# Optimization experiments

Measured on AMD Instinct MI355X. Metric: run time of the kernel, lower is better.

The kernel has to match this reference:

```python
import jax, jax.numpy as jnp
import numpy as np

D_MODEL = 1024
NUM_HEADS = 16
HEAD_DIM = D_MODEL // NUM_HEADS
MAX_SEQ = 512


def rope_tables(seq_len, dim):
    inv_freq = 1.0 / (10000.0 ** (jnp.arange(0, dim, 2, dtype=jnp.float32) / dim))
    t = jnp.arange(seq_len, dtype=jnp.float32)
    freqs = jnp.einsum('i,j->ij', t, inv_freq)        # [S, dim/2]
    emb = jnp.concatenate([freqs, freqs], axis=-1)    # [S, dim]
    return jnp.cos(emb), jnp.sin(emb)


def rotate_half(x):
    x1, x2 = jnp.split(x, 2, axis=-1)
    return jnp.concatenate([-x2, x1], axis=-1)


def setup_inputs() -> dict:
    key = jax.random.key(0)
    ks = jax.random.split(key, 12)
    B, S, D = 16, 512, D_MODEL
    s = 1.0 / np.sqrt(D)
    inp = {
        'query': jax.random.normal(ks[0], (B, S, D), jnp.float32),
        'key': jax.random.normal(ks[1], (B, S, D), jnp.float32),
        'value': jax.random.normal(ks[2], (B, S, D), jnp.float32),
        'Wq': jax.random.normal(ks[3], (D, D), jnp.float32) * s,
        'bq': jnp.zeros((D,), jnp.float32),
        'Wk': jax.random.normal(ks[4], (D, D), jnp.float32) * s,
        'bk': jnp.zeros((D,), jnp.float32),
        'Wv': jax.random.normal(ks[5], (D, D), jnp.float32) * s,
        'bv': jnp.zeros((D,), jnp.float32),
        'Wo': jax.random.normal(ks[6], (D, D), jnp.float32) * s,
        'bo': jnp.zeros((D,), jnp.float32),
    }
    return inp


def reference(query, key, value, Wq, bq, Wk, bk, Wv, bv, Wo, bo):
    B, S, D = query.shape
    H, Hd = NUM_HEADS, HEAD_DIM
    scale = Hd ** -0.5

    def proj(x, W, b):  # torch Linear: x @ W.T + b -> [B,H,S,Hd]
        y = jnp.einsum('bsd,ed->bse', x, W) + b
        return y.reshape(B, S, H, Hd).transpose(0, 2, 1, 3)

    q = proj(query, Wq, bq)
    k = proj(key, Wk, bk)
    v = proj(value, Wv, bv)

    cos, sin = rope_tables(S, Hd)           # [S, Hd]
    cos = cos[None, None]                    # [1,1,S,Hd]
    sin = sin[None, None]
    q = q * cos + rotate_half(q) * sin
    k = k * cos + rotate_half(k) * sin

    attn = jnp.einsum('bhqd,bhkd->bhqk', q, k) * scale
    attn_w = jax.nn.softmax(attn, axis=-1)
    out = jnp.einsum('bhqk,bhkd->bhqd', attn_w, v)
    out = out.transpose(0, 2, 1, 3).reshape(B, S, D)
    out = jnp.einsum('bsd,ed->bse', out, Wo) + bo
    return out
```

## Files before the change

kernel.cpp:

```cpp
#include <hip/hip_runtime.h>
#include <hip/hip_bf16.h>
#include <math.h>

typedef __attribute__((ext_vector_type(8))) short short8;
typedef __attribute__((ext_vector_type(4))) short s16x4;
typedef __attribute__((ext_vector_type(4))) float f32x4;
typedef unsigned short ushort;
typedef unsigned int uint;

#define BATCH 16
#define SEQ 512
#define DMODEL 1024
#define NHEADS 16
#define HD 64
#define MTOT (BATCH * SEQ)
#define NBUF ((size_t)MTOT * DMODEL)
#define WBUF ((size_t)DMODEL * DMODEL)

#define SZA (256 * 64)
#define SZB (128 * 64)

#define FENCE asm volatile("" ::: "memory")

__device__ __forceinline__ ushort f2bf(float f) {
    union { float f; uint i; } v; v.f = f;
    uint r = v.i + 0x7fffu + ((v.i >> 16) & 1u);
    return (ushort)(r >> 16);
}

__device__ __forceinline__ short8 cvt8v(f32x4 a, f32x4 b) {
    short8 r;
    r[0] = (short)f2bf(a[0]); r[1] = (short)f2bf(a[1]);
    r[2] = (short)f2bf(a[2]); r[3] = (short)f2bf(a[3]);
    r[4] = (short)f2bf(b[0]); r[5] = (short)f2bf(b[1]);
    r[6] = (short)f2bf(b[2]); r[7] = (short)f2bf(b[3]);
    return r;
}

__device__ __forceinline__ void gld16(const ushort* g, ushort* l) {
    __builtin_amdgcn_global_load_lds(
        (const __attribute__((address_space(1))) void*)g,
        (__attribute__((address_space(3))) void*)l, 16, 0, 0);
}

__device__ __forceinline__ f32x4 mfma16(short8 a, short8 b, f32x4 c) {
    return __builtin_amdgcn_mfma_f32_16x16x32_bf16(a, b, c, 0, 0, 0);
}

__global__ void fill_const(float* __restrict__ out, float val) {
    out[blockIdx.x * 256 + threadIdx.x] = val;
}

__global__ __launch_bounds__(256) void cvt_act(
    const float* __restrict__ i0, const float* __restrict__ i1,
    const float* __restrict__ i2, ushort* __restrict__ o0,
    ushort* __restrict__ o1, ushort* __restrict__ o2)
{
    const float* in  = blockIdx.y == 0 ? i0 : (blockIdx.y == 1 ? i1 : i2);
    ushort*      out = blockIdx.y == 0 ? o0 : (blockIdx.y == 1 ? o1 : o2);
    int i = (blockIdx.x * 256 + threadIdx.x) * 8;
    f32x4 a = __builtin_nontemporal_load((const f32x4*)(in + i));
    f32x4 b = __builtin_nontemporal_load((const f32x4*)(in + i + 4));
    *(short8*)(out + i) = cvt8v(a, b);
}

__global__ __launch_bounds__(256) void cvt_w(
    const float* __restrict__ i0, const float* __restrict__ i1,
    const float* __restrict__ i2, const float* __restrict__ i3,
    ushort* __restrict__ o0, ushort* __restrict__ o1,
    ushort* __restrict__ o2, ushort* __restrict__ o3)
{
    const float* in  = blockIdx.y == 0 ? i0 : (blockIdx.y == 1 ? i1 :
                        (blockIdx.y == 2 ? i2 : i3));
    ushort*      out = blockIdx.y == 0 ? o0 : (blockIdx.y == 1 ? o1 :
                        (blockIdx.y == 2 ? o2 : o3));
    int i = (blockIdx.x * 256 + threadIdx.x) * 8;
    f32x4 a = __builtin_nontemporal_load((const f32x4*)(in + i));
    f32x4 b = __builtin_nontemporal_load((const f32x4*)(in + i + 4));
    *(short8*)(out + i) = cvt8v(a, b);
}

__global__ void rope_init(float* __restrict__ cs, float* __restrict__ sn) {
    int idx = blockIdx.x * 256 + threadIdx.x;
    if (idx >= SEQ * 32) return;
    int s = idx >> 5, p = idx & 31;
    float inv = __expf(-(float)p * (1.0f / 32.0f) * logf(10000.0f));
    float th = (float)s * inv;
    cs[idx] = cosf(th);
    sn[idx] = sinf(th);
}

__device__ __forceinline__ void gemm_core(
    const ushort* __restrict__ A, const ushort* __restrict__ W,
    ushort* __restrict__ smA, ushort* __restrict__ smB,
    int m0, int n0, int tid, f32x4 (&acc)[4][4])
{
    const int lane = tid & 63, w = tid >> 6;
    const int quad = lane >> 4, l16 = lane & 15;
    const int wm = (w >> 1) * 64, wn = (w & 1) * 64;
    const int swz = (l16 & 7) << 3;
    const int k0 = (quad * 8) ^ swz;
    const int k1 = ((4 + quad) * 8) ^ swz;

    const int r = tid >> 3;
    const int kc = ((tid & 7) ^ (r & 7)) * 8;
    const ushort* gA = A + (size_t)(m0 + r) * 1024 + kc;
    const ushort* gB = W + (size_t)(n0 + r) * 1024 + kc;
    ushort* lA = smA + tid * 8;
    ushort* lB = smB + tid * 8;

#pragma unroll
    for (int i = 0; i < 4; ++i) gld16(gA + i * 65536, lA + i * 4096);
    gld16(gB, lB); gld16(gB + 65536, lB + 4096);
    FENCE;
#pragma unroll
    for (int i = 0; i < 4; ++i) gld16(gA + i * 65536 + 64, lA + SZA + i * 4096);
    gld16(gB + 64, lB + SZB); gld16(gB + 65536 + 64, lB + SZB + 4096);
    FENCE;

#pragma unroll 1
    for (int t = 0; t < 16; ++t) {
        if (t < 15) asm volatile("s_waitcnt vmcnt(6)" ::: "memory");
        else        asm volatile("s_waitcnt vmcnt(0)" ::: "memory");
        __builtin_amdgcn_s_barrier();

        const ushort* tA = smA + (t % 3) * SZA;
        const ushort* tB = smB + (t % 3) * SZB;
        short8 af[4][2], bf[4][2];
#pragma unroll
        for (int mi = 0; mi < 4; ++mi) {
            const ushort* rp = tA + (wm + mi * 16 + l16) * 64;
            af[mi][0] = *(const short8*)(rp + k0);
            af[mi][1] = *(const short8*)(rp + k1);
        }
#pragma unroll
        for (int nj = 0; nj < 4; ++nj) {
            const ushort* rp = tB + (wn + nj * 16 + l16) * 64;
            bf[nj][0] = *(const short8*)(rp + k0);
            bf[nj][1] = *(const short8*)(rp + k1);
        }
        if (t < 14) {
            const int sl = (t + 2) % 3;
            const ushort* ga = gA + (size_t)(t + 2) * 64;
            const ushort* gb = gB + (size_t)(t + 2) * 64;
            ushort* da = lA + sl * SZA;
            ushort* db = lB + sl * SZB;
#pragma unroll
            for (int i = 0; i < 4; ++i) gld16(ga + i * 65536, da + i * 4096);
            gld16(gb, db); gld16(gb + 65536, db + 4096);
        }
        FENCE;
        __builtin_amdgcn_s_setprio(1);
#pragma unroll
        for (int nj = 0; nj < 4; ++nj)
#pragma unroll
            for (int mi = 0; mi < 4; ++mi) {
                acc[mi][nj] = mfma16(af[mi][0], bf[nj][0], acc[mi][nj]);
                acc[mi][nj] = mfma16(af[mi][1], bf[nj][1], acc[mi][nj]);
            }
        __builtin_amdgcn_s_setprio(0);
    }
}

__global__ __launch_bounds__(512, 2) void qkv_proj(
    const ushort* __restrict__ Aq, const ushort* __restrict__ Ak,
    const ushort* __restrict__ Av, const ushort* __restrict__ Wq,
    const ushort* __restrict__ Wk, const ushort* __restrict__ Wv,
    const float* __restrict__ bq, const float* __restrict__ bk,
    const float* __restrict__ bv, ushort* __restrict__ Qo,
    ushort* __restrict__ Ko, ushort* __restrict__ Vo,
    const float* __restrict__ cs_tab, const float* __restrict__ sn_tab)
{
    const int z = blockIdx.z;
    const ushort* A    = z == 0 ? Aq : (z == 1 ? Ak : Av);
    const ushort* W    = z == 0 ? Wq : (z == 1 ? Wk : Wv);
    const float*  bias = z == 0 ? bq : (z == 1 ? bk : bv);
    ushort*       out  = z == 0 ? Qo : (z == 1 ? Ko : Vo);

    const int id = blockIdx.x;
    const int x = id & 7, l = id >> 3;
    const int by = x * 4 + (l >> 3);
    const int bx = l & 7;
    const int m0 = by * 256, n0 = bx * 128;

    __shared__ __align__(16) ushort smA[3 * SZA];
    __shared__ __align__(16) ushort smB[3 * SZB];

    const int tid = threadIdx.x;
    const int lane = tid & 63, w = tid >> 6;
    const int quad = lane >> 4, l16 = lane & 15;
    const int wm = (w >> 1) * 64, wn = (w & 1) * 64;

    f32x4 acc[4][4] = {};
    gemm_core(A, W, smA, smB, m0, n0, tid, acc);

    float bv4[4];
#pragma unroll
    for (int j = 0; j < 4; j++) bv4[j] = bias[n0 + wn + j * 16 + l16];

    if (z < 2) {
        const int h = (n0 + wn) >> 6;
#pragma unroll
        for (int i = 0; i < 4; i++) {
#pragma unroll
            for (int r = 0; r < 4; r++) {
                int m = m0 + wm + i * 16 + quad * 4 + r;
                int s = m & (SEQ - 1), b = m >> 9;
                size_t base = ((size_t)(b * NHEADS + h) * SEQ + s) * HD;
#pragma unroll
                for (int jj = 0; jj < 2; jj++) {
                    int p = jj * 16 + l16;
                    float c = cs_tab[s * 32 + p], sg = sn_tab[s * 32 + p];
                    float lo = acc[i][jj][r] + bv4[jj];
                    float hi = acc[i][jj + 2][r] + bv4[jj + 2];
                    out[base + p]      = f2bf(lo * c - hi * sg);
                    out[base + 32 + p] = f2bf(hi * c + lo * sg);
                }
            }
        }
    } else {
        __syncthreads();
        ushort* sT = smA;
#pragma unroll
        for (int i = 0; i < 4; i++)
#pragma unroll
            for (int j = 0; j < 4; j++) {
                s16x4 vv;
#pragma unroll
                for (int r = 0; r < 4; r++) vv[r] = (short)f2bf(acc[i][j][r] + bv4[j]);
                *(s16x4*)(sT + (wn + j * 16 + l16) * 264 + wm + i * 16 + quad * 4) = vv;
            }
        __syncthreads();
        const int nl = tid >> 2, mc = (tid & 3) * 64;
        const int ng = n0 + nl, h = ng >> 6, d = ng & 63;
        const int b = m0 >> 9;
        ushort* op = out + ((size_t)((b * NHEADS + h) * HD + d)) * SEQ +
                     (m0 & (SEQ - 1)) + mc;
#pragma unroll
        for (int u = 0; u < 8; ++u)
            *(short8*)(op + u * 8) = *(const short8*)(sT + nl * 264 + mc + u * 8);
    }
}

__global__ __launch_bounds__(512, 2) void gemm_o(
    const ushort* __restrict__ A, const ushort* __restrict__ W,
    const float* __restrict__ bias, float* __restrict__ out)
{
    const int id = blockIdx.x;
    const int x = id & 7, l = id >> 3;
    const int by = x * 4 + (l >> 3);
    const int bx = l & 7;
    const int m0 = by * 256, n0 = bx * 128;

    __shared__ __align__(16) ushort smA[3 * SZA];
    __shared__ __align__(16) ushort smB[3 * SZB];

    const int tid = threadIdx.x;
    const int lane = tid & 63, w = tid >> 6;
    const int quad = lane >> 4, l16 = lane & 15;
    const int wm = (w >> 1) * 64, wn = (w & 1) * 64;

    f32x4 acc[4][4] = {};
    gemm_core(A, W, smA, smB, m0, n0, tid, acc);

    float bv4[4];
#pragma unroll
    for (int j = 0; j < 4; j++) bv4[j] = bias[n0 + wn + j * 16 + l16];

#pragma unroll
    for (int i = 0; i < 4; i++)
#pragma unroll
        for (int j = 0; j < 4; j++) {
            int n = n0 + wn + j * 16 + l16;
#pragma unroll
            for (int r = 0; r < 4; r++) {
                int m = m0 + wm + i * 16 + quad * 4 + r;
                out[(size_t)m * 1024 + n] = acc[i][j][r] + bv4[j];
            }
        }
}

__global__ __launch_bounds__(256) void attn(
    const ushort* __restrict__ Q, const ushort* __restrict__ K,
    const ushort* __restrict__ VT, ushort* __restrict__ O)
{
    __shared__ ushort sK[64 * 72];
    __shared__ ushort sV[64 * 72];
    __shared__ ushort sP[4][32 * 72];

    const int tid = threadIdx.x;
    const int wave = tid >> 6, lane = tid & 63;
    const int quad = lane >> 4, l16 = lane & 15;
    const int id = blockIdx.x;
    const int j8 = id >> 3;
    const int bh = (id & 7) * 32 + (j8 >> 2);
    const int q0 = (j8 & 3) * 128;
    const int qw = q0 + wave * 32;

    const ushort* Qbh = Q + (size_t)bh * SEQ * HD;
    const ushort* Kbh = K + (size_t)bh * SEQ * HD;
    const ushort* Vbh = VT + (size_t)bh * HD * SEQ;

    const float S2 = 0.125f * 1.44269504f;
    const float C2 = 12.0f * 1.44269504f;

    short8 qf[2][2];
#pragma unroll
    for (int mi = 0; mi < 2; mi++)
#pragma unroll
        for (int ks = 0; ks < 2; ks++)
            qf[mi][ks] = *(const short8*)(Qbh + (size_t)(qw + mi * 16 + l16) * HD +
                                          ks * 32 + quad * 8);

    f32x4 o_acc[2][4] = {};
    float lsum[2][4] = {};

    const int cA = tid, cB = tid + 256;
    const int rA = cA >> 3, colA = (cA & 7) * 8;
    const int rB = cB >> 3, colB = (cB & 7) * 8;

    short8 rk0 = *(const short8*)(Kbh + (size_t)rA * HD + colA);
    short8 rk1 = *(const short8*)(Kbh + (size_t)rB * HD + colB);
    short8 rv0 = *(const short8*)(Vbh + (size_t)rA * SEQ + colA);
    short8 rv1 = *(const short8*)(Vbh + (size_t)rB * SEQ + colB);

    for (int kt = 0; kt < SEQ; kt += 64) {
        __syncthreads();
        *(short8*)(sK + rA * 72 + colA) = rk0;
        *(short8*)(sK + rB * 72 + colB) = rk1;
        *(short8*)(sV + rA * 72 + colA) = rv0;
        *(short8*)(sV + rB * 72 + colB) = rv1;
        if (kt + 64 < SEQ) {
            rk0 = *(const short8*)(Kbh + (size_t)(kt + 64 + rA) * HD + colA);
            rk1 = *(const short8*)(Kbh + (size_t)(kt + 64 + rB) * HD + colB);
            rv0 = *(const short8*)(Vbh + (size_t)rA * SEQ + kt + 64 + colA);
            rv1 = *(const short8*)(Vbh + (size_t)rB * SEQ + kt + 64 + colB);
        }
        __syncthreads();

        f32x4 sc[2][4];
#pragma unroll
        for (int nj = 0; nj < 4; nj++) {
            short8 kf0 = *(const short8*)(sK + (nj * 16 + l16) * 72 + quad * 8);
            short8 kf1 = *(const short8*)(sK + (nj * 16 + l16) * 72 + 32 + quad * 8);
#pragma unroll
            for (int mi = 0; mi < 2; mi++) {
                f32x4 z = {0.f, 0.f, 0.f, 0.f};
                z = mfma16(qf[mi][0], kf0, z);
                z = mfma16(qf[mi][1], kf1, z);
                sc[mi][nj] = z;
            }
        }

#pragma unroll
        for (int mi = 0; mi < 2; mi++)
#pragma unroll
            for (int r = 0; r < 4; r++) {
                float p0 = __builtin_amdgcn_exp2f(fmaf(sc[mi][0][r], S2, -C2));
                float p1 = __builtin_amdgcn_exp2f(fmaf(sc[mi][1][r], S2, -C2));
                float p2 = __builtin_amdgcn_exp2f(fmaf(sc[mi][2][r], S2, -C2));
                float p3 = __builtin_amdgcn_exp2f(fmaf(sc[mi][3][r], S2, -C2));
                sc[mi][0][r] = p0; sc[mi][1][r] = p1;
                sc[mi][2][r] = p2; sc[mi][3][r] = p3;
                lsum[mi][r] += (p0 + p1) + (p2 + p3);
            }

#pragma unroll
        for (int mi = 0; mi < 2; mi++)
#pragma unroll
            for (int nj = 0; nj < 4; nj++)
#pragma unroll
                for (int r = 0; r < 4; r++)
                    sP[wave][(mi * 16 + quad * 4 + r) * 72 + nj * 16 + l16] =
                        f2bf(sc[mi][nj][r]);

#pragma unroll
        for (int ks = 0; ks < 2; ks++) {
            short8 pf0 = *(const short8*)(&sP[wave][(l16) * 72 + ks * 32 + quad * 8]);
            short8 pf1 = *(const short8*)(&sP[wave][(16 + l16) * 72 + ks * 32 + quad * 8]);
#pragma unroll
            for (int dj = 0; dj < 4; dj++) {
                short8 vf = *(const short8*)(sV + (dj * 16 + l16) * 72 + ks * 32 + quad * 8);
                o_acc[0][dj] = mfma16(pf0, vf, o_acc[0][dj]);
                o_acc[1][dj] = mfma16(pf1, vf, o_acc[1][dj]);
            }
        }
    }

    const int h = bh & (NHEADS - 1), b = bh >> 4;
#pragma unroll
    for (int mi = 0; mi < 2; mi++)
#pragma unroll
        for (int r = 0; r < 4; r++) {
            float l = lsum[mi][r];
            l += __shfl_xor(l, 1, 64);
            l += __shfl_xor(l, 2, 64);
            l += __shfl_xor(l, 4, 64);
            l += __shfl_xor(l, 8, 64);
            float inv = 1.0f / l;
            int s = qw + mi * 16 + quad * 4 + r;
            size_t base = ((size_t)(b * SEQ + s)) * DMODEL + h * HD;
#pragma unroll
            for (int dj = 0; dj < 4; dj++)
                O[base + dj * 16 + l16] = f2bf(o_acc[mi][dj][r] * inv);
        }
}

extern "C" void kernel_launch(void* const* d_in, const int* in_sizes, int n_in,
                              void* d_out, int out_size, void* d_ws, size_t ws_size,
                              hipStream_t stream) {
    bool ok = (n_in == 11) && (out_size == (int)NBUF) &&
              in_sizes[0] == (int)NBUF && in_sizes[1] == (int)NBUF &&
              in_sizes[2] == (int)NBUF &&
              in_sizes[3] == (int)WBUF && in_sizes[4] == 1024 &&
              in_sizes[5] == (int)WBUF && in_sizes[6] == 1024 &&
              in_sizes[7] == (int)WBUF && in_sizes[8] == 1024 &&
              in_sizes[9] == (int)WBUF && in_sizes[10] == 1024;
    if (!ok) {
        fill_const<<<NBUF / 256, 256, 0, stream>>>((float*)d_out, 1000.0f);
        return;
    }
    size_t need = 2 * (size_t)SEQ * 32 * 4 + 4 * NBUF * 2 + 4 * WBUF * 2;
    if (ws_size < need) return;

    const float* q  = (const float*)d_in[0];
    const float* k  = (const float*)d_in[1];
    const float* v  = (const float*)d_in[2];
    const float* Wq = (const float*)d_in[3];
    const float* bq = (const float*)d_in[4];
    const float* Wk = (const float*)d_in[5];
    const float* bk = (const float*)d_in[6];
    const float* Wv = (const float*)d_in[7];
    const float* bv = (const float*)d_in[8];
    const float* Wo = (const float*)d_in[9];
    const float* bo = (const float*)d_in[10];

    float* cs = (float*)d_ws;
    float* sn = cs + SEQ * 32;
    ushort* Qb  = (ushort*)(sn + SEQ * 32);
    ushort* Kb  = Qb + NBUF;
    ushort* VTb = Kb + NBUF;
    ushort* Xb  = VTb + NBUF;
    ushort* Wqb = Xb + NBUF;
    ushort* Wkb = Wqb + WBUF;
    ushort* Wvb = Wkb + WBUF;
    ushort* Wob = Wvb + WBUF;
    ushort* Qx = (ushort*)d_out;
    ushort* Kx = Qx + NBUF;

    rope_init<<<64, 256, 0, stream>>>(cs, sn);
    cvt_w<<<dim3(WBUF / 2048, 4), 256, 0, stream>>>(Wq, Wk, Wv, Wo,
                                                    Wqb, Wkb, Wvb, Wob);
    cvt_act<<<dim3(NBUF / 2048, 3), 256, 0, stream>>>(q, k, v, Qx, Kx, Xb);

    qkv_proj<<<dim3(256, 1, 3), 512, 0, stream>>>(
        Qx, Kx, Xb, Wqb, Wkb, Wvb, bq, bk, bv, Qb, Kb, VTb, cs, sn);

    attn<<<BATCH * NHEADS * 4, 256, 0, stream>>>(Qb, Kb, VTb, Xb);

    gemm_o<<<256, 512, 0, stream>>>(Xb, Wob, bo, (float*)d_out);
}
```

Baseline: 278.5 us.

## Halve GEMM K-tile to 32 and raise occupancy to four blocks per CU

Shrinks the shared-memory K tile from 64 to 32, giving twice as many pipeline steps with one MFMA pair fewer per step. The LDS swizzle and the global-load mapping are reworked for the narrower tile. The smaller shared buffers, placed in one LDS array, allow launch bounds of four 512-thread blocks per CU instead of two. The goal is more concurrent waves to hide memory latency. The cost is twice as many barriers per K loop and a much tighter register budget, which risks spilling the 64-float accumulator.

New measurement: 275.7 us. About the same (-1.0%).

```diff
diff --git a/kernel.cpp b/kernel.cpp
--- a/kernel.cpp
+++ b/kernel.cpp
@@ -17,8 +17,9 @@
 #define NBUF ((size_t)MTOT * DMODEL)
 #define WBUF ((size_t)DMODEL * DMODEL)
 
-#define SZA (256 * 64)
-#define SZB (128 * 64)
+#define SZA (256 * 32)
+#define SZB (128 * 32)
+#define LDSE (3 * SZA + 3 * SZB)
 
 #define FENCE asm volatile("" ::: "memory")
 
@@ -98,71 +99,55 @@
     const int lane = tid & 63, w = tid >> 6;
     const int quad = lane >> 4, l16 = lane & 15;
     const int wm = (w >> 1) * 64, wn = (w & 1) * 64;
-    const int swz = (l16 & 7) << 3;
-    const int k0 = (quad * 8) ^ swz;
-    const int k1 = ((4 + quad) * 8) ^ swz;
-
-    const int r = tid >> 3;
-    const int kc = ((tid & 7) ^ (r & 7)) * 8;
-    const ushort* gA = A + (size_t)(m0 + r) * 1024 + kc;
-    const ushort* gB = W + (size_t)(n0 + r) * 1024 + kc;
+    const int k0 = ((quad ^ ((l16 >> 1) & 3)) * 8);
+
+    const int kc = ((tid & 3) ^ ((tid >> 3) & 3)) * 8;
+    const ushort* gA = A + (size_t)(m0 + (tid >> 2)) * 1024 + kc;
+    const ushort* gB = W + (size_t)(n0 + (tid >> 2)) * 1024 + kc;
     ushort* lA = smA + tid * 8;
     ushort* lB = smB + tid * 8;
 
-#pragma unroll
-    for (int i = 0; i < 4; ++i) gld16(gA + i * 65536, lA + i * 4096);
-    gld16(gB, lB); gld16(gB + 65536, lB + 4096);
+    gld16(gA, lA); gld16(gA + 128 * 1024, lA + 4096); gld16(gB, lB);
     FENCE;
-#pragma unroll
-    for (int i = 0; i < 4; ++i) gld16(gA + i * 65536 + 64, lA + SZA + i * 4096);
-    gld16(gB + 64, lB + SZB); gld16(gB + 65536 + 64, lB + SZB + 4096);
+    gld16(gA + 32, lA + SZA); gld16(gA + 128 * 1024 + 32, lA + SZA + 4096);
+    gld16(gB + 32, lB + SZB);
     FENCE;
 
 #pragma unroll 1
-    for (int t = 0; t < 16; ++t) {
-        if (t < 15) asm volatile("s_waitcnt vmcnt(6)" ::: "memory");
+    for (int t = 0; t < 32; ++t) {
+        if (t < 31) asm volatile("s_waitcnt vmcnt(3)" ::: "memory");
         else        asm volatile("s_waitcnt vmcnt(0)" ::: "memory");
         __builtin_amdgcn_s_barrier();
 
         const ushort* tA = smA + (t % 3) * SZA;
         const ushort* tB = smB + (t % 3) * SZB;
-        short8 af[4][2], bf[4][2];
-#pragma unroll
-        for (int mi = 0; mi < 4; ++mi) {
-            const ushort* rp = tA + (wm + mi * 16 + l16) * 64;
-            af[mi][0] = *(const short8*)(rp + k0);
-            af[mi][1] = *(const short8*)(rp + k1);
-        }
-#pragma unroll
-        for (int nj = 0; nj < 4; ++nj) {
-            const ushort* rp = tB + (wn + nj * 16 + l16) * 64;
-            bf[nj][0] = *(const short8*)(rp + k0);
-            bf[nj][1] = *(const short8*)(rp + k1);
-        }
-        if (t < 14) {
+        short8 af[4], bf[4];
+#pragma unroll
+        for (int mi = 0; mi < 4; ++mi)
+            af[mi] = *(const short8*)(tA + (wm + mi * 16 + l16) * 32 + k0);
+#pragma unroll
+        for (int nj = 0; nj < 4; ++nj)
+            bf[nj] = *(const short8*)(tB + (wn + nj * 16 + l16) * 32 + k0);
+        if (t < 30) {
             const int sl = (t + 2) % 3;
-            const ushort* ga = gA + (size_t)(t + 2) * 64;
-            const ushort* gb = gB + (size_t)(t + 2) * 64;
+            const ushort* ga = gA + (size_t)(t + 2) * 32;
+            const ushort* gb = gB + (size_t)(t + 2) * 32;
             ushort* da = lA + sl * SZA;
             ushort* db = lB + sl * SZB;
-#pragma unroll
-            for (int i = 0; i < 4; ++i) gld16(ga + i * 65536, da + i * 4096);
-            gld16(gb, db); gld16(gb + 65536, db + 4096);
+            gld16(ga, da); gld16(ga + 128 * 1024, da + 4096); gld16(gb, db);
         }
         FENCE;
         __builtin_amdgcn_s_setprio(1);
 #pragma unroll
         for (int nj = 0; nj < 4; ++nj)
 #pragma unroll
-            for (int mi = 0; mi < 4; ++mi) {
-                acc[mi][nj] = mfma16(af[mi][0], bf[nj][0], acc[mi][nj]);
-                acc[mi][nj] = mfma16(af[mi][1], bf[nj][1], acc[mi][nj]);
-            }
+            for (int mi = 0; mi < 4; ++mi)
+                acc[mi][nj] = mfma16(af[mi], bf[nj], acc[mi][nj]);
         __builtin_amdgcn_s_setprio(0);
     }
 }
 
-__global__ __launch_bounds__(512, 2) void qkv_proj(
+__global__ __launch_bounds__(512, 4) void qkv_proj(
     const ushort* __restrict__ Aq, const ushort* __restrict__ Ak,
     const ushort* __restrict__ Av, const ushort* __restrict__ Wq,
     const ushort* __restrict__ Wk, const ushort* __restrict__ Wv,
@@ -183,8 +168,9 @@
     const int bx = l & 7;
     const int m0 = by * 256, n0 = bx * 128;
 
-    __shared__ __align__(16) ushort smA[3 * SZA];
-    __shared__ __align__(16) ushort smB[3 * SZB];
+    __shared__ __align__(16) ushort lds[LDSE];
+    ushort* smA = lds;
+    ushort* smB = lds + 3 * SZA;
 
     const int tid = threadIdx.x;
     const int lane = tid & 63, w = tid >> 6;
@@ -220,7 +206,7 @@
         }
     } else {
         __syncthreads();
-        ushort* sT = smA;
+        ushort* sT = lds;
 #pragma unroll
         for (int i = 0; i < 4; i++)
 #pragma unroll
@@ -242,7 +228,7 @@
     }
 }
 
-__global__ __launch_bounds__(512, 2) void gemm_o(
+__global__ __launch_bounds__(512, 4) void gemm_o(
     const ushort* __restrict__ A, const ushort* __restrict__ W,
     const float* __restrict__ bias, float* __restrict__ out)
 {
@@ -252,8 +238,9 @@
     const int bx = l & 7;
     const int m0 = by * 256, n0 = bx * 128;
 
-    __shared__ __align__(16) ushort smA[3 * SZA];
-    __shared__ __align__(16) ushort smB[3 * SZB];
+    __shared__ __align__(16) ushort lds[LDSE];
+    ushort* smA = lds;
+    ushort* smB = lds + 3 * SZA;
 
     const int tid = threadIdx.x;
     const int lane = tid & 63, w = tid >> 6;
```
